# Optimization experiments

Hardware: AMD Instinct MI355X
Metric: run time of the kernel (lower is better)

## Reference

```python
import jax, jax.numpy as jnp
import numpy as np

B, C, P, H, W = 8, 256, 64, 64, 64


def conv2d(x, w, b, pad):
    y = jax.lax.conv_general_dilated(
        x, w, window_strides=(1, 1), padding=[(pad, pad), (pad, pad)],
        dimension_numbers=("NCHW", "OIHW", "NCHW"))
    return y + b[None, :, None, None]


def setup_inputs() -> dict:
    key = jax.random.key(0)
    ks = jax.random.split(key, 9)
    x = jax.random.normal(ks[0], (B, C, H, W), dtype=jnp.float32)
    # conv weights, OIHW layout; scale ~ kaiming-ish
    w_top = jax.random.normal(ks[1], (P, C, 1, 1), jnp.float32) * (1.0 / np.sqrt(C))
    b_top = jnp.zeros((P,), jnp.float32)
    w_center = jax.random.normal(ks[2], (P, C, 1, 1), jnp.float32) * (1.0 / np.sqrt(C))
    b_center = jnp.zeros((P,), jnp.float32)
    w_bottom = jax.random.normal(ks[3], (C, C, 3, 3), jnp.float32) * (1.0 / np.sqrt(9 * C))
    b_bottom = jnp.zeros((C,), jnp.float32)
    w_out = jax.random.normal(ks[4], (C, C, 3, 3), jnp.float32) * (1.0 / np.sqrt(9 * C))
    b_out = jnp.zeros((C,), jnp.float32)
    return {"x": x, "w_top": w_top, "b_top": b_top, "w_center": w_center,
            "b_center": b_center, "w_bottom": w_bottom, "b_bottom": b_bottom,
            "w_out": w_out, "b_out": b_out}


def reference(x, w_top, b_top, w_center, b_center, w_bottom, b_bottom, w_out, b_out):
    b, c, h, w = x.shape
    hw = h * w
    x_top = conv2d(x, w_top, b_top, 0).reshape(b, -1, hw)          # [B, P, HW]
    x_center = conv2d(x, w_center, b_center, 0).reshape(b, -1, hw)  # [B, P, HW]
    x_center = jnp.swapaxes(x_center, 1, 2)                          # [B, HW, P]
    x_bottom = conv2d(x, w_bottom, b_bottom, 1).reshape(b, c, hw)
    x_bottom = jnp.swapaxes(x_bottom, 1, 2)                          # [B, HW, C]
    sp_map = jnp.einsum("bnp,bpm->bnm", x_center, x_top)            # [B, HW, HW]
    # NOTE: softmax is GLOBAL over the flattened HW*HW map per batch element,
    # not per-row (faithful to original Softmax(dim=1) on view(bsize, -1)).
    sp_map = jax.nn.softmax(sp_map.reshape(b, -1), axis=1).reshape(b, hw, hw)
    sp_map = jnp.einsum("bnm,bmc->bnc", sp_map, x_bottom)           # [B, HW, C]
    # NOTE: original does .reshape(b, C, h, w) on a [B, HW, C] tensor (no
    # transpose) -- replicate that exact memory reinterpretation.
    sp_map = sp_map.reshape(b, c, h, w)
    return conv2d(x + sp_map, w_out, b_out, 1)
```

## Files before the change

kernel.cpp:

```cpp
#include <hip/hip_runtime.h>
#include <hip/hip_bf16.h>
#include <type_traits>

constexpr int B_ = 8, C_ = 256, P_ = 64, H_ = 64, W_ = 64, HW_ = 4096;

typedef __attribute__((ext_vector_type(8))) short short8;
typedef __attribute__((ext_vector_type(4))) short short4v;
typedef __attribute__((ext_vector_type(4))) float f32x4;

__device__ __forceinline__ short bfbits(float f) {
    __hip_bfloat16 h = __float2bfloat16(f);
    return *reinterpret_cast<short*>(&h);
}
__device__ __forceinline__ float bf2f(short s) {
    __hip_bfloat16 h = *reinterpret_cast<__hip_bfloat16*>(&s);
    return (float)h;
}

#define GLL16(gsrc, ldst)                                                      \
    __builtin_amdgcn_global_load_lds(                                         \
        (const __attribute__((address_space(1))) void*)(gsrc),                \
        (__attribute__((address_space(3))) void*)(ldst), 16, 0, 0)


__global__ __launch_bounds__(256) void k_prep_w(
    const float* __restrict__ w, short8* __restrict__ wbP)
{
    const int idx = blockIdx.x * 256 + threadIdx.x;
    const int lane = idx & 63, cot = (idx >> 6) & 15;
    const int cb = (idx >> 10) & 7, tap = idx >> 13;
    const int lm = lane & 15, lq = lane >> 4;
    const int co = cot * 16 + lm, ci0 = cb * 32 + lq * 8;
    short8 v;
#pragma unroll
    for (int k = 0; k < 8; ++k)
        v[k] = bfbits(w[(co * 256 + ci0 + k) * 9 + tap]);
    wbP[idx] = v;
}

__global__ __launch_bounds__(256) void k_prep_w1(
    const float* __restrict__ wt, const float* __restrict__ wc,
    short8* __restrict__ w1P)
{
    const int idx = blockIdx.x * 256 + threadIdx.x;
    const int lane = idx & 63, kc = (idx >> 6) & 7;
    const int pt = (idx >> 9) & 3, conv = idx >> 11;
    const int lm = lane & 15, lq = lane >> 4;
    const float* w = conv ? wc : wt;
    const float* wp = w + (pt * 16 + lm) * C_ + kc * 32 + lq * 8;
    short8 vh, vl;
#pragma unroll
    for (int k = 0; k < 8; ++k) {
        const float v = wp[k];
        const short h = bfbits(v);
        vh[k] = h;
        vl[k] = bfbits(v - bf2f(h));
    }
    const size_t o = (((size_t)(conv * 4 + pt) * 8 + kc) * 2) * 64 + lane;
    w1P[o] = vh;
    w1P[o + 64] = vl;
}

__global__ __launch_bounds__(256) void k_cvt_bf16(
    const float* __restrict__ x, short8* __restrict__ xB)
{
    const size_t i = ((size_t)blockIdx.x * 256 + threadIdx.x) * 16;
    short8 o[2];
#pragma unroll
    for (int q = 0; q < 2; ++q) {
#pragma unroll
        for (int j = 0; j < 2; ++j) {
            const float4 v = *reinterpret_cast<const float4*>(&x[i + q * 8 + j * 4]);
            o[q][j * 4 + 0] = bfbits(v.x);
            o[q][j * 4 + 1] = bfbits(v.y);
            o[q][j * 4 + 2] = bfbits(v.z);
            o[q][j * 4 + 3] = bfbits(v.w);
        }
    }
    short8* dp = (short8*)&xB[i >> 3];
    dp[0] = o[0];
    dp[1] = o[1];
}

__global__ __launch_bounds__(256) void k_pack_xb(
    const __hip_bfloat16* __restrict__ xb, short8* __restrict__ xbP)
{
    const int tid = blockIdx.x * 256 + threadIdx.x;
    const int lane = tid & 63, wid = tid >> 6;
    const int ct = wid & 15, g = (wid >> 4) & 127, b = wid >> 11;
    const int c = ct * 16 + (lane >> 2);
    const int mo = g * 32 + (lane & 3) * 8;
    const short8 v = *reinterpret_cast<const short8*>(
        &xb[((size_t)(b * 256 + c)) * HW_ + mo]);
    xbP[(size_t)wid * 64 + (lane & 3) * 16 + (lane >> 2)] = v;
}

__global__ __launch_bounds__(256) void k_conv1x1_mfma(
    const float* __restrict__ x, const short8* __restrict__ w1P,
    const float* __restrict__ b_top, const float* __restrict__ b_cen,
    short4v* __restrict__ xtPh, short4v* __restrict__ xtPl,
    short4v* __restrict__ xcPh, short4v* __restrict__ xcPl)
{
    const int b = blockIdx.y;
    const int t = threadIdx.x, wv = t >> 6, lane = t & 63;
    const int lm = lane & 15, lq = lane >> 4;
    const int nt = blockIdx.x * 4 + wv;
    const float* xp = x + (size_t)b * C_ * HW_ + nt * 16 + lm;

    f32x4 acc[2][4];
#pragma unroll
    for (int i = 0; i < 2; ++i)
#pragma unroll
        for (int j = 0; j < 4; ++j) acc[i][j] = f32x4{0.f, 0.f, 0.f, 0.f};

    for (int kc = 0; kc < 8; ++kc) {
        short8 bh, bl;
#pragma unroll
        for (int k = 0; k < 8; ++k) {
            const float v = xp[(size_t)(kc * 32 + lq * 8 + k) * HW_];
            const short h = bfbits(v);
            bh[k] = h;
            bl[k] = bfbits(v - bf2f(h));
        }
#pragma unroll
        for (int conv = 0; conv < 2; ++conv)
#pragma unroll
            for (int pt = 0; pt < 4; ++pt) {
                const size_t o =
                    (((size_t)(conv * 4 + pt) * 8 + kc) * 2) * 64 + lane;
                const short8 ah = w1P[o];
                const short8 al = w1P[o + 64];
                f32x4 a = acc[conv][pt];
                a = __builtin_amdgcn_mfma_f32_16x16x32_bf16(ah, bh, a, 0, 0, 0);
                a = __builtin_amdgcn_mfma_f32_16x16x32_bf16(ah, bl, a, 0, 0, 0);
                a = __builtin_amdgcn_mfma_f32_16x16x32_bf16(al, bh, a, 0, 0, 0);
                acc[conv][pt] = a;
            }
    }

#pragma unroll
    for (int conv = 0; conv < 2; ++conv) {
        const float* bias = conv ? b_cen : b_top;
        short4v* oh = conv ? xcPh : xtPh;
        short4v* ol = conv ? xcPl : xtPl;
#pragma unroll
        for (int pt = 0; pt < 4; ++pt) {
            const int kc = pt >> 1;
            const int tl = (pt & 1) * 2 + (lq >> 1);
            const size_t c16 = ((size_t)(b * 256 + nt) * 2 + kc) * 64 + tl * 16 + lm;
            short4v vh, vl;
#pragma unroll
            for (int r = 0; r < 4; ++r) {
                const float v = acc[conv][pt][r] + bias[pt * 16 + lq * 4 + r];
                const short h = bfbits(v);
                vh[r] = h;
                vl[r] = bfbits(v - bf2f(h));
            }
            oh[c16 * 2 + (lq & 1)] = vh;
            ol[c16 * 2 + (lq & 1)] = vl;
        }
    }
}

template <typename OT>
__global__ __launch_bounds__(512, 4) void k_conv3x3_mfma(
    const short* __restrict__ xin, const short8* __restrict__ wbP,
    const float* __restrict__ bias, OT* __restrict__ out)
{
    __shared__ __align__(16) short Xs[3][66][40];
    const int lin = blockIdx.x;
    const int b = lin & 7, h = lin >> 3;
    const int t = threadIdx.x;
    const int wave = t >> 6, lane = t & 63;
    const int lm = lane & 15, lq = lane >> 4;
    const int cobase = wave * 32;
    const int cot0 = wave * 2;

    f32x4 acc[4][2];
#pragma unroll
    for (int i = 0; i < 4; ++i)
#pragma unroll
        for (int j = 0; j < 2; ++j) acc[i][j] = f32x4{0.f, 0.f, 0.f, 0.f};

    if (t < 192) {
        const int r = t >> 6, cc = t & 31, side = (t >> 5) & 1;
        Xs[r][side ? 65 : 0][cc] = 0;
    }

    const short* xbase = xin + (size_t)b * C_ * HW_;

    for (int cb = 0; cb < 8; ++cb) {
        const int ci0 = cb * 32;
        __syncthreads();
#pragma unroll
        for (int it = 0; it < 3; ++it) {
            const int idx = it * 512 + t;
            const int r = idx >> 9, ci = (idx >> 4) & 31, wq = idx & 15;
            const int hh = h + r - 1;
            short4v v = {0, 0, 0, 0};
            if (hh >= 0 && hh < H_)
                v = *reinterpret_cast<const short4v*>(
                    &xbase[(size_t)(ci0 + ci) * HW_ + hh * W_ + wq * 4]);
            Xs[r][1 + wq * 4 + 0][ci] = v[0];
            Xs[r][1 + wq * 4 + 1][ci] = v[1];
            Xs[r][1 + wq * 4 + 2][ci] = v[2];
            Xs[r][1 + wq * 4 + 3][ci] = v[3];
        }
        __syncthreads();

#pragma unroll 3
        for (int tap = 0; tap < 9; ++tap) {
            const int dh = tap / 3;
            const int dw = tap % 3;
            const short8* wp = wbP + ((size_t)(tap * 8 + cb)) * 1024 + lane;
            short8 af[2];
            af[0] = wp[(cot0 + 0) * 64];
            af[1] = wp[(cot0 + 1) * 64];
            short8 bf[4];
#pragma unroll
            for (int nt = 0; nt < 4; ++nt)
                bf[nt] = *reinterpret_cast<const short8*>(
                    &Xs[dh][nt * 16 + lm + dw][lq * 8]);
#pragma unroll
            for (int nt = 0; nt < 4; ++nt)
#pragma unroll
                for (int ct = 0; ct < 2; ++ct)
                    acc[nt][ct] = __builtin_amdgcn_mfma_f32_16x16x32_bf16(
                        af[ct], bf[nt], acc[nt][ct], 0, 0, 0);
        }
    }

#pragma unroll
    for (int nt = 0; nt < 4; ++nt) {
        const int pos = h * W_ + nt * 16 + lm;
#pragma unroll
        for (int ct = 0; ct < 2; ++ct) {
            const int co = cobase + ct * 16 + lq * 4;
#pragma unroll
            for (int r = 0; r < 4; ++r) {
                const float v = acc[nt][ct][r] + bias[co + r];
                if constexpr (std::is_same<OT, __hip_bfloat16>::value)
                    out[((size_t)(b * C_ + co + r)) * HW_ + pos] = __float2bfloat16(v);
                else
                    out[((size_t)(b * C_ + co + r)) * HW_ + pos] = v;
            }
        }
    }
}

__global__ __launch_bounds__(512, 2) void k_attn_mfma(
    const short8* __restrict__ xtPh, const short8* __restrict__ xtPl,
    const short8* __restrict__ xcPh, const short8* __restrict__ xcPl,
    const short8* __restrict__ xbP, float* __restrict__ O,
    float* __restrict__ Z)
{
    extern __shared__ __align__(16) char smem[];
    short8* XTs = (short8*)smem;
    short8* XBs = (short8*)(smem + 32768);
    short8* Ps8 = (short8*)(smem + 98304);
    short4v* Ps4 = (short4v*)(smem + 98304);
    float* zred = (float*)(smem + 114688);

    const int lin = blockIdx.x;
    const int b = lin & 7, nblk = lin >> 3;
    const int n0 = nblk * 128;

    const int t = threadIdx.x, wv = t >> 6, lane = t & 63;
    const int lm = lane & 15, lq = lane >> 4;
    const int mh = wv >> 2, nq2 = wv & 3;
    const int nq = wv >> 2, cq = wv & 3;

    short8 cB2[2][2][2];
#pragma unroll
    for (int ntile = 0; ntile < 2; ++ntile) {
        const int gt = nblk * 8 + nq2 * 2 + ntile;
        const size_t base = ((size_t)(b * 256 + gt) * 2) * 64 + lane;
        cB2[ntile][0][0] = xcPh[base];
        cB2[ntile][1][0] = xcPh[base + 64];
        cB2[ntile][0][1] = xcPl[base];
        cB2[ntile][1][1] = xcPl[base + 64];
    }
    asm volatile("s_waitcnt vmcnt(0)" ::: "memory");

    auto stage = [&](int smt, int bufi) {
        short8* XT = XTs + bufi * 1024;
        short8* XB = XBs + bufi * 2048;
        const size_t abase = ((size_t)(b * 512 + smt * 8)) * 64;
#pragma unroll
        for (int k = 0; k < 2; ++k) {
            const int c = wv * 2 + k, ms = c >> 2, part = c & 3;
            const short8* src = (part < 2 ? xtPh : xtPl)
                                + abase + ms * 128 + (part & 1) * 64 + lane;
            GLL16(src, XT + c * 64);
        }
        const size_t p8 = ((size_t)(b * 2048 + smt * 32)) * 64;
#pragma unroll
        for (int k = 0; k < 4; ++k) {
            const int e = k * 512 + wv * 64;
            GLL16(xbP + p8 + e + lane, XB + e);
        }
    };
    stage(0, 0);

    f32x4 acc[4][4];
#pragma unroll
    for (int i = 0; i < 4; ++i)
#pragma unroll
        for (int jj = 0; jj < 4; ++jj) acc[i][jj] = f32x4{0.f, 0.f, 0.f, 0.f};
    float zp = 0.f;

    for (int mt = 0; mt < 64; ++mt) {
        const int cur = mt & 1;
        asm volatile("s_waitcnt vmcnt(4)" ::: "memory");
        __builtin_amdgcn_sched_barrier(0);
        __builtin_amdgcn_s_barrier();
        __builtin_amdgcn_sched_barrier(0);
        stage((mt + 1) & 63, cur ^ 1);

        const short8* XT = XTs + cur * 1024;
#pragma unroll
        for (int ms2 = 0; ms2 < 2; ++ms2) {
            const int ms = mh * 2 + ms2;
            const short8 aH0 = XT[(ms * 4 + 0) * 64 + lane];
            const short8 aH1 = XT[(ms * 4 + 1) * 64 + lane];
            const short8 aL0 = XT[(ms * 4 + 2) * 64 + lane];
            const short8 aL1 = XT[(ms * 4 + 3) * 64 + lane];
#pragma unroll
            for (int ntile = 0; ntile < 2; ++ntile) {
                f32x4 s = {0.f, 0.f, 0.f, 0.f};
                __builtin_amdgcn_s_setprio(1);
                s = __builtin_amdgcn_mfma_f32_16x16x32_bf16(aH0, cB2[ntile][0][0], s, 0, 0, 0);
                s = __builtin_amdgcn_mfma_f32_16x16x32_bf16(aH1, cB2[ntile][1][0], s, 0, 0, 0);
                s = __builtin_amdgcn_mfma_f32_16x16x32_bf16(aH0, cB2[ntile][0][1], s, 0, 0, 0);
                s = __builtin_amdgcn_mfma_f32_16x16x32_bf16(aH1, cB2[ntile][1][1], s, 0, 0, 0);
                s = __builtin_amdgcn_mfma_f32_16x16x32_bf16(aL0, cB2[ntile][0][0], s, 0, 0, 0);
                s = __builtin_amdgcn_mfma_f32_16x16x32_bf16(aL1, cB2[ntile][1][0], s, 0, 0, 0);
                __builtin_amdgcn_s_setprio(0);
                const float e0 = __expf(s[0]), e1 = __expf(s[1]);
                const float e2 = __expf(s[2]), e3 = __expf(s[3]);
                zp += (e0 + e1) + (e2 + e3);
                short4v pk = { bfbits(e0), bfbits(e1), bfbits(e2), bfbits(e3) };
                const int T = nq2 * 2 + ntile;
                const int lqp = (ms & 1) * 2 + (lq >> 1);
                Ps4[(((T * 2 + mh) * 64) + lqp * 16 + lm) * 2 + (lq & 1)] = pk;
            }
        }
        asm volatile("s_waitcnt vmcnt(6) lgkmcnt(0)" ::: "memory");
        __builtin_amdgcn_sched_barrier(0);
        __builtin_amdgcn_s_barrier();
        __builtin_amdgcn_sched_barrier(0);

        const short8* XB = XBs + cur * 2048;
        short8 vb0[4], vb1[4];
#pragma unroll
        for (int q4 = 0; q4 < 4; ++q4) {
            const int ct = cq * 4 + q4;
            vb0[q4] = XB[ct * 64 + lane];
            vb1[q4] = XB[1024 + ct * 64 + lane];
        }
#pragma unroll
        for (int nt2 = 0; nt2 < 4; ++nt2) {
            const int T = nq * 4 + nt2;
            const short8 pa0 = Ps8[(T * 2 + 0) * 64 + lane];
            const short8 pa1 = Ps8[(T * 2 + 1) * 64 + lane];
            __builtin_amdgcn_s_setprio(1);
#pragma unroll
            for (int q4 = 0; q4 < 4; ++q4) {
                acc[nt2][q4] = __builtin_amdgcn_mfma_f32_16x16x32_bf16(
                    pa0, vb0[q4], acc[nt2][q4], 0, 0, 0);
                acc[nt2][q4] = __builtin_amdgcn_mfma_f32_16x16x32_bf16(
                    pa1, vb1[q4], acc[nt2][q4], 0, 0, 0);
            }
            __builtin_amdgcn_s_setprio(0);
        }
    }

#pragma unroll
    for (int o = 32; o > 0; o >>= 1) zp += __shfl_down(zp, o, 64);
    if (lane == 0) zred[wv] = zp;
    __syncthreads();
    if (t == 0) {
        float zs = 0.f;
#pragma unroll
        for (int wvi = 0; wvi < 8; ++wvi) zs += zred[wvi];
        atomicAdd(&Z[b], zs);
    }

#pragma unroll
    for (int nt2 = 0; nt2 < 4; ++nt2) {
#pragma unroll
        for (int q4 = 0; q4 < 4; ++q4) {
            const int c = cq * 64 + q4 * 16 + lm;
#pragma unroll
            for (int r = 0; r < 4; ++r) {
                const int n = n0 + (nq * 4 + nt2) * 16 + lq * 4 + r;
                O[((size_t)b * HW_ + n) * C_ + c] = acc[nt2][q4][r];
            }
        }
    }
}

__global__ __launch_bounds__(256) void k_add_bf16(
    const float* __restrict__ x, const float* __restrict__ o,
    const float* __restrict__ Z, short4v* __restrict__ yB)
{
    const int bidx = blockIdx.x;
    const float invZ = 1.0f / Z[bidx >> 10];
    const size_t i = ((size_t)bidx * 256 + threadIdx.x) * 4;
    const float4 a = *reinterpret_cast<const float4*>(&x[i]);
    const float4 b = *reinterpret_cast<const float4*>(&o[i]);
    short4v r{bfbits(fmaf(b.x, invZ, a.x)), bfbits(fmaf(b.y, invZ, a.y)),
              bfbits(fmaf(b.z, invZ, a.z)), bfbits(fmaf(b.w, invZ, a.w))};
    yB[i >> 2] = r;
}

extern "C" void kernel_launch(void* const* d_in, const int* in_sizes, int n_in,
                              void* d_out, int out_size, void* d_ws, size_t ws_size,
                              hipStream_t stream)
{
    const float* x   = (const float*)d_in[0];
    const float* wt  = (const float*)d_in[1];
    const float* bt  = (const float*)d_in[2];
    const float* wc  = (const float*)d_in[3];
    const float* bc  = (const float*)d_in[4];
    const float* wbo = (const float*)d_in[5];
    const float* bbo = (const float*)d_in[6];
    const float* wo  = (const float*)d_in[7];
    const float* bo  = (const float*)d_in[8];
    float* out = (float*)d_out;

    uint8_t* w8 = (uint8_t*)d_ws;
    const size_t MB = 1u << 20;
    short8* xtPh = (short8*)(w8);
    short8* xtPl = (short8*)(w8 + 4 * MB);
    short8* xcPh = (short8*)(w8 + 8 * MB);
    short8* xcPl = (short8*)(w8 + 12 * MB);
    short8* W1   = (short8*)(w8 + 16 * MB);
    __hip_bfloat16* xbB = (__hip_bfloat16*)(w8 + 16 * MB);
    short8* xbP  = (short8*)(w8 + 32 * MB);
    float*  O    = (float*)(w8 + 48 * MB);
    short8* Wb1  = (short8*)(w8 + 48 * MB);
    short8* xB   = (short8*)(w8 + 64 * MB);
    short8* Wb2  = (short8*)(w8 + 32 * MB);
    short4v* yB  = (short4v*)(w8 + 16 * MB);
    float*  Z    = (float*)(w8 + 80 * MB);

    hipMemsetAsync(Z, 0, B_ * sizeof(float), stream);
    k_prep_w<<<dim3(288), 256, 0, stream>>>(wbo, Wb1);
    k_prep_w1<<<dim3(16), 256, 0, stream>>>(wt, wc, W1);
    k_cvt_bf16<<<dim3(2048), 256, 0, stream>>>(x, xB);
    k_conv1x1_mfma<<<dim3(64, 8), 256, 0, stream>>>(
        x, W1, bt, bc, (short4v*)xtPh, (short4v*)xtPl,
        (short4v*)xcPh, (short4v*)xcPl);
    k_conv3x3_mfma<__hip_bfloat16><<<dim3(512), 512, 0, stream>>>(
        (const short*)xB, Wb1, bbo, xbB);
    k_pack_xb<<<dim3(4096), 256, 0, stream>>>(xbB, xbP);
    k_attn_mfma<<<dim3(256), dim3(512), 114720, stream>>>(xtPh, xtPl, xcPh, xcPl,
                                                          xbP, O, Z);
    k_prep_w<<<dim3(288), 256, 0, stream>>>(wo, Wb2);
    k_add_bf16<<<dim3(8192), 256, 0, stream>>>(x, O, Z, yB);
    k_conv3x3_mfma<float><<<dim3(512), 512, 0, stream>>>(
        (const short*)yB, Wb2, bo, out);
}
```

Measured before the change: 364.5 us.

## Compute two output rows per conv3x3 block to reuse the input halo

The 3x3 convolution kernel now uses 1024 threads per block and produces two output rows per block instead of one, staging four input rows in shared memory instead of three. Each group of eight waves handles one output row, so the shared halo rows are loaded once for both rows. This cuts global input traffic per output row and halves the grid size. The trade-off is larger blocks with fewer blocks in flight and possibly lower occupancy. Weight fragments are still reloaded per wave.

```diff
diff --git a/kernel.cpp b/kernel.cpp
--- a/kernel.cpp
+++ b/kernel.cpp
@@ -163,18 +163,17 @@
 }
 
 template <typename OT>
-__global__ __launch_bounds__(512, 4) void k_conv3x3_mfma(
+__global__ __launch_bounds__(1024, 4) void k_conv3x3_mfma(
     const short* __restrict__ xin, const short8* __restrict__ wbP,
     const float* __restrict__ bias, OT* __restrict__ out)
 {
-    __shared__ __align__(16) short Xs[3][66][40];
+    __shared__ __align__(16) short Xs[4][66][40];
     const int lin = blockIdx.x;
-    const int b = lin & 7, h = lin >> 3;
+    const int b = lin & 7, hp = lin >> 3;
     const int t = threadIdx.x;
     const int wave = t >> 6, lane = t & 63;
     const int lm = lane & 15, lq = lane >> 4;
-    const int cobase = wave * 32;
-    const int cot0 = wave * 2;
+    const int nq = wave >> 3, ch = wave & 7;
 
     f32x4 acc[4][2];
 #pragma unroll
@@ -182,7 +181,7 @@
 #pragma unroll
         for (int j = 0; j < 2; ++j) acc[i][j] = f32x4{0.f, 0.f, 0.f, 0.f};
 
-    if (t < 192) {
+    if (t < 256) {
         const int r = t >> 6, cc = t & 31, side = (t >> 5) & 1;
         Xs[r][side ? 65 : 0][cc] = 0;
     }
@@ -193,10 +192,10 @@
         const int ci0 = cb * 32;
         __syncthreads();
 #pragma unroll
-        for (int it = 0; it < 3; ++it) {
-            const int idx = it * 512 + t;
+        for (int it = 0; it < 2; ++it) {
+            const int idx = it * 1024 + t;
             const int r = idx >> 9, ci = (idx >> 4) & 31, wq = idx & 15;
-            const int hh = h + r - 1;
+            const int hh = hp * 2 + r - 1;
             short4v v = {0, 0, 0, 0};
             if (hh >= 0 && hh < H_)
                 v = *reinterpret_cast<const short4v*>(
@@ -212,33 +211,34 @@
         for (int tap = 0; tap < 9; ++tap) {
             const int dh = tap / 3;
             const int dw = tap % 3;
+            const int slot = nq + dh;
             const short8* wp = wbP + ((size_t)(tap * 8 + cb)) * 1024 + lane;
             short8 af[2];
-            af[0] = wp[(cot0 + 0) * 64];
-            af[1] = wp[(cot0 + 1) * 64];
+            af[0] = wp[(ch * 2 + 0) * 64];
+            af[1] = wp[(ch * 2 + 1) * 64];
             short8 bf[4];
 #pragma unroll
-            for (int nt = 0; nt < 4; ++nt)
-                bf[nt] = *reinterpret_cast<const short8*>(
-                    &Xs[dh][nt * 16 + lm + dw][lq * 8]);
-#pragma unroll
-            for (int nt = 0; nt < 4; ++nt)
+            for (int wt = 0; wt < 4; ++wt)
+                bf[wt] = *reinterpret_cast<const short8*>(
+                    &Xs[slot][wt * 16 + lm + dw][lq * 8]);
+#pragma unroll
+            for (int wt = 0; wt < 4; ++wt)
 #pragma unroll
                 for (int ct = 0; ct < 2; ++ct)
-                    acc[nt][ct] = __builtin_amdgcn_mfma_f32_16x16x32_bf16(
-                        af[ct], bf[nt], acc[nt][ct], 0, 0, 0);
-        }
-    }
-
-#pragma unroll
-    for (int nt = 0; nt < 4; ++nt) {
-        const int pos = h * W_ + nt * 16 + lm;
+                    acc[wt][ct] = __builtin_amdgcn_mfma_f32_16x16x32_bf16(
+                        af[ct], bf[wt], acc[wt][ct], 0, 0, 0);
+        }
+    }
+
+#pragma unroll
+    for (int wt = 0; wt < 4; ++wt) {
+        const int pos = (hp * 2 + nq) * W_ + wt * 16 + lm;
 #pragma unroll
         for (int ct = 0; ct < 2; ++ct) {
-            const int co = cobase + ct * 16 + lq * 4;
+            const int co = ch * 32 + ct * 16 + lq * 4;
 #pragma unroll
             for (int r = 0; r < 4; ++r) {
-                const float v = acc[nt][ct][r] + bias[co + r];
+                const float v = acc[wt][ct][r] + bias[co + r];
                 if constexpr (std::is_same<OT, __hip_bfloat16>::value)
                     out[((size_t)(b * C_ + co + r)) * HW_ + pos] = __float2bfloat16(v);
                 else
@@ -452,13 +452,13 @@
     k_conv1x1_mfma<<<dim3(64, 8), 256, 0, stream>>>(
         x, W1, bt, bc, (short4v*)xtPh, (short4v*)xtPl,
         (short4v*)xcPh, (short4v*)xcPl);
-    k_conv3x3_mfma<__hip_bfloat16><<<dim3(512), 512, 0, stream>>>(
+    k_conv3x3_mfma<__hip_bfloat16><<<dim3(256), 1024, 0, stream>>>(
         (const short*)xB, Wb1, bbo, xbB);
     k_pack_xb<<<dim3(4096), 256, 0, stream>>>(xbB, xbP);
     k_attn_mfma<<<dim3(256), dim3(512), 114720, stream>>>(xtPh, xtPl, xcPh, xcPl,
                                                           xbP, O, Z);
     k_prep_w<<<dim3(288), 256, 0, stream>>>(wo, Wb2);
     k_add_bf16<<<dim3(8192), 256, 0, stream>>>(x, O, Z, yB);
-    k_conv3x3_mfma<float><<<dim3(512), 512, 0, stream>>>(
+    k_conv3x3_mfma<float><<<dim3(256), 1024, 0, stream>>>(
         (const short*)yB, Wb2, bo, out);
 }
```

Result: no change. 362.0 us (-0.7%).
